# Kernel tuning notes

Hardware: AMD Instinct MI355X
Metric: run time of the kernel (lower is better)

The kernel has to match this reference:

```python
import jax, jax.numpy as jnp
import numpy as np

DIM = 64
WS = 8    # window_size
SS = 4    # shift_size


def _conv(x, w, pad, groups=1):
    return jax.lax.conv_general_dilated(
        x, w, (1, 1), ((pad, pad), (pad, pad)),
        dimension_numbers=('NCHW', 'OIHW', 'NCHW'),
        feature_group_count=groups)


def _window_partition(x, ws):
    # x: (B, C, H, W) -> (B*Hn*Wn, C, ws, ws), with bottom/right padding
    B, C, H, W = x.shape
    pb = (-H) % ws
    pr = (-W) % ws
    x = jnp.pad(x, ((0, 0), (0, 0), (0, pb), (0, pr)))
    Hp, Wp = H + pb, W + pr
    x = x.reshape(B, C, Hp // ws, ws, Wp // ws, ws).transpose(0, 1, 2, 4, 3, 5)
    return x.reshape(-1, C, ws, ws)


def _window_reverse(wins, ws, H, W):
    pb = (-H) % ws
    pr = (-W) % ws
    Hp, Wp = H + pb, W + pr
    B = wins.shape[0] // ((Hp // ws) * (Wp // ws))
    x = wins.reshape(B, -1, Hp // ws, Wp // ws, ws, ws).transpose(0, 1, 2, 4, 3, 5)
    x = x.reshape(B, -1, Hp, Wp)
    return x[:, :, :H, :W]


def _create_mask(H, W, ws, ss):
    # Swin-style additive mask, computed statically with numpy
    Hp = int(np.ceil(H / ws)) * ws
    Wp = int(np.ceil(W / ws)) * ws
    m = np.zeros((Hp, Wp), dtype=np.float32)
    slices = (slice(0, -ws), slice(-ws, -ss), slice(-ss, None))
    cnt = 0
    for hs in slices:
        for wsl in slices:
            m[hs, wsl] = cnt
            cnt += 1
    mw = m.reshape(Hp // ws, ws, Wp // ws, ws).transpose(0, 2, 1, 3).reshape(-1, ws * ws)
    diff = mw[:, None, :] - mw[:, :, None]
    return jnp.asarray(np.where(diff != 0, -100.0, 0.0).astype(np.float32))


def _l2norm(x):
    # matches torch F.normalize(dim=-1, eps=1e-12)
    return x / jnp.maximum(jnp.linalg.norm(x, axis=-1, keepdims=True), 1e-12)


def _win_attn(xw, w_qkv, w_dw, w_proj, ws, mask, b):
    # xw: (N, C, ws, ws) windows
    C = xw.shape[1]
    qkv = _conv(_conv(xw, w_qkv, 0), w_dw, 1, groups=3 * C)
    q, k, v = jnp.split(qkv, 3, axis=1)
    N = q.shape[0]
    hw = ws * ws
    q = _l2norm(q.reshape(N, C, hw))
    k = _l2norm(k.reshape(N, C, hw))
    v = v.reshape(N, C, hw)
    attn = jnp.einsum('nci,ncj->nij', q, k) / ws  # (N, hw, hw)
    if mask is not None:
        attn = (attn.reshape(b, -1, hw, hw) + mask[None]).reshape(-1, hw, hw)
    attn = jax.nn.softmax(attn, axis=-1)
    out = jnp.einsum('nci,nij->ncj', v, attn).reshape(N, C, ws, ws)
    return _conv(out, w_proj, 1)


def _forward(x, w_qkv0, w_dw0, w_proj0, w_qkv1, w_dw1, w_proj1):
    b, c, h, w = x.shape
    # pass 1: unshifted windows
    xw = _window_partition(x, WS)
    out = _win_attn(xw, w_qkv0, w_dw0, w_proj0, WS, None, b)
    out = _window_reverse(out, WS, h, w)
    # pass 2: shifted windows with Swin mask
    shift = jnp.roll(out, (-SS, -SS), axis=(2, 3))
    sw = _window_partition(shift, WS)
    mask = _create_mask(h, w, WS, SS)
    out = _win_attn(sw, w_qkv1, w_dw1, w_proj1, WS, mask, b)
    out = _window_reverse(out, WS, h, w)
    return jnp.roll(out, (SS, SS), axis=(2, 3))


def setup_inputs() -> dict:
    key = jax.random.key(0)
    ks = jax.random.split(key, 7)
    C = DIM
    s = 0.05
    return {
        'x': jax.random.normal(ks[0], (8, C, 256, 256), jnp.float32),
        'w_qkv0': jax.random.normal(ks[1], (3 * C, C, 1, 1), jnp.float32) * s,
        'w_dw0': jax.random.normal(ks[2], (3 * C, 1, 3, 3), jnp.float32) * s,
        'w_proj0': jax.random.normal(ks[3], (C, C, 3, 3), jnp.float32) * s,
        'w_qkv1': jax.random.normal(ks[4], (3 * C, C, 1, 1), jnp.float32) * s,
        'w_dw1': jax.random.normal(ks[5], (3 * C, 1, 3, 3), jnp.float32) * s,
        'w_proj1': jax.random.normal(ks[6], (C, C, 3, 3), jnp.float32) * s,
    }


def reference(x, w_qkv0, w_dw0, w_proj0, w_qkv1, w_dw1, w_proj1):
    return _forward(x, w_qkv0, w_dw0, w_proj0, w_qkv1, w_dw1, w_proj1)
```

## Files before the change

kernel.cpp:

```cpp
#include <hip/hip_runtime.h>


typedef __attribute__((ext_vector_type(8))) short bf8;
typedef __attribute__((ext_vector_type(4))) float f32x4;
#define MFMA(a, b, c) __builtin_amdgcn_mfma_f32_16x16x32_bf16(a, b, c, 0, 0, 0)

__device__ __forceinline__ int xkey(int p) { return ((p >> 3) ^ p) & 7; }
__device__ __forceinline__ int xswz(int p, int c) { return p * 64 + (c ^ (xkey(p) << 3)); }
__device__ __forceinline__ int sswz(int ch, int p) {
    return ch * 64 + (p ^ (((ch >> 1) & 7) << 2));
}
__device__ __forceinline__ int jswz(int ch, int p) {
    return ch * 64 + (p ^ (((ch >> 1) & 7) << 3));
}

__device__ __forceinline__ unsigned cvtpk(float a, float b) {
    unsigned r;
    asm("v_cvt_pk_bf16_f32 %0, %1, %2" : "=v"(r) : "v"(a), "v"(b));
    return r;
}

__device__ __forceinline__ void bsplit(float f, short& h, short& l) {
    unsigned u = __float_as_uint(f);
    unsigned hb = (u + 0x7FFFu + ((u >> 16) & 1u)) >> 16;
    float hf = __uint_as_float(hb << 16);
    float r = f - hf;
    unsigned u2 = __float_as_uint(r);
    unsigned lb = (u2 + 0x7FFFu + ((u2 >> 16) & 1u)) >> 16;
    h = (short)hb; l = (short)lb;
}
__device__ __forceinline__ void bsplit2(float a, float b, unsigned& hw, unsigned& lw) {
    hw = cvtpk(a, b);
    float ra = a - __uint_as_float(hw << 16);
    float rb = b - __uint_as_float(hw & 0xFFFF0000u);
    lw = cvtpk(ra, rb);
}

__global__ void k_fq(const float* __restrict__ wq, short* __restrict__ oh, short* __restrict__ ol) {
    int bx = blockIdx.x;
    int kk = bx / 12, tt = bx % 12;
    int tid = threadIdx.x;
    int lane = tid >> 3, j = tid & 7;
    int oc = tt * 16 + (lane & 15);
    int ic = kk * 32 + ((lane >> 4) << 3) + j;
    short h, l; bsplit(wq[oc * 64 + ic], h, l);
    oh[bx * 512 + tid] = h; ol[bx * 512 + tid] = l;
}
__global__ void k_fp(const float* __restrict__ wp, short* __restrict__ oh, short* __restrict__ ol) {
    int bx = blockIdx.x;
    int tap = bx >> 3, kk = (bx >> 2) & 1, tt = bx & 3;
    int tid = threadIdx.x;
    int lane = tid >> 3, j = tid & 7;
    int oc = tt * 16 + (lane & 15);
    int ic = kk * 32 + ((lane >> 4) << 3) + j;
    short h, l; bsplit(wp[(oc * 64 + ic) * 9 + tap], h, l);
    oh[bx * 512 + tid] = h; ol[bx * 512 + tid] = l;
}

__device__ __forceinline__ void dw_one(const float* scr, const float* wd,
                                       int ch, int row, float o[8]) {
    float w9[9];
    #pragma unroll
    for (int tp = 0; tp < 9; ++tp) w9[tp] = wd[tp];
    float e[3][10];
    #pragma unroll
    for (int k3 = 0; k3 < 3; ++k3) {
        int rr = row - 1 + k3;
        e[k3][0] = 0.f; e[k3][9] = 0.f;
        if ((unsigned)rr < 8u) {
            float4 a = *(const float4*)&scr[sswz(ch, rr * 8)];
            float4 b = *(const float4*)&scr[sswz(ch, rr * 8 + 4)];
            e[k3][1] = a.x; e[k3][2] = a.y; e[k3][3] = a.z; e[k3][4] = a.w;
            e[k3][5] = b.x; e[k3][6] = b.y; e[k3][7] = b.z; e[k3][8] = b.w;
        } else {
            #pragma unroll
            for (int q2 = 1; q2 < 9; ++q2) e[k3][q2] = 0.f;
        }
    }
    #pragma unroll
    for (int s = 0; s < 8; ++s) {
        float a = 0.f;
        #pragma unroll
        for (int k3 = 0; k3 < 3; ++k3)
            #pragma unroll
            for (int dx = 0; dx < 3; ++dx)
                a = fmaf(w9[k3 * 3 + dx], e[k3][s + dx], a);
        o[s] = a;
    }
}

__device__ __forceinline__ float norm8(const float d[8]) {
    float ss = 0.f;
    #pragma unroll
    for (int s = 0; s < 8; ++s) ss = fmaf(d[s], d[s], ss);
    ss += __shfl_xor(ss, 1); ss += __shfl_xor(ss, 2); ss += __shfl_xor(ss, 4);
    return fmaxf(sqrtf(ss), 1e-12f);
}

__device__ __forceinline__ void p2_chunk32(const short* XTh, const short* XTl,
                                           const short* bqh, const short* bql,
                                           float* scr, int chunk,
                                           int mh, int nh, int col, int quad, int qo8, int lane)
{
    f32x4 acc[2];
    #pragma unroll
    for (int mt = 0; mt < 2; ++mt) acc[mt] = (f32x4){0.f, 0.f, 0.f, 0.f};
    #pragma unroll
    for (int kk = 0; kk < 2; ++kk) {
        bf8 Ah[2], Al[2];
        #pragma unroll
        for (int mt = 0; mt < 2; ++mt) {
            int row = (mh * 2 + mt) * 16 + col;
            int ad = row * 64 + ((kk * 32 + qo8) ^ (xkey(row) << 3));
            Ah[mt] = *(const bf8*)&XTh[ad];
            Al[mt] = *(const bf8*)&XTl[ad];
        }
        int tt = chunk * 2 + nh;
        bf8 Bh = *(const bf8*)&bqh[((kk * 12 + tt) * 64 + lane) * 8];
        bf8 Bl = *(const bf8*)&bql[((kk * 12 + tt) * 64 + lane) * 8];
        #pragma unroll
        for (int mt = 0; mt < 2; ++mt) {
            acc[mt] = MFMA(Ah[mt], Bh, acc[mt]);
            acc[mt] = MFMA(Ah[mt], Bl, acc[mt]);
            acc[mt] = MFMA(Al[mt], Bh, acc[mt]);
        }
    }
    #pragma unroll
    for (int mt = 0; mt < 2; ++mt) {
        int ocl = nh * 16 + col;
        int p0 = (mh * 2 + mt) * 16 + quad * 4;
        *(f32x4*)&scr[sswz(ocl, p0)] = acc[mt];
    }
}

__global__ __launch_bounds__(256, 4)
void k_fused(const float* __restrict__ in,
             const short* __restrict__ bqh, const short* __restrict__ bql,
             const float* __restrict__ wdw,
             const short* __restrict__ bph, const short* __restrict__ bpl,
             float* __restrict__ out, int shift, int use_mask, int roll)
{
    __shared__ __align__(16) char smem[40960];
    short* XTh = (short*)smem;
    short* XTl = (short*)(smem + 8192);
    short* kTh = (short*)(smem + 16384);
    short* kTl = (short*)(smem + 24576);
    short* vbh = kTh;
    short* vbl = kTl;
    float* scr = (float*)(smem + 32768);
    short* PTh = (short*)(smem + 32768);
    short* PTl = (short*)(smem + 36864);
    float* projo = (float*)(smem + 16384);

    const int tid = threadIdx.x, lane = tid & 63, wv = tid >> 6;
    const int col = lane & 15, quad = lane >> 4, qo8 = quad * 8;
    const int mh = wv & 1, nh = wv >> 1;
    const int ch = tid >> 3, rrow = tid & 7;
    const int n = blockIdx.x;
    const int b = n >> 10, c = (n >> 4) & 63, t = n & 15;
    const size_t base = ((size_t)(b * 64 + c)) << 16;

    #pragma unroll
    for (int k = 0; k < 16; k += 2) {
        int o0 = tid + k * 256, o1 = o0 + 256;
        int hi0 = o0 >> 11, r0 = (o0 >> 8) & 7, lo0 = (o0 >> 3) & 31, s0 = o0 & 7;
        int hi1 = o1 >> 11, r1 = (o1 >> 8) & 7, lo1 = (o1 >> 3) & 31, s1 = o1 & 7;
        float v0 = in[base + (size_t)(((t * 16 + hi0 * 8 + r0) + shift) & 255) * 256
                           + (((lo0 * 8 + s0) + shift) & 255)];
        float v1 = in[base + (size_t)(((t * 16 + hi1 * 8 + r1) + shift) & 255) * 256
                           + (((lo1 * 8 + s1) + shift) & 255)];
        unsigned hw, lw; bsplit2(v0, v1, hw, lw);
        int ad0 = xswz(r0 * 8 + s0, hi0 * 32 + lo0);
        int ad1 = xswz(r1 * 8 + s1, hi1 * 32 + lo1);
        XTh[ad0] = (short)hw; XTh[ad1] = (short)(hw >> 16);
        XTl[ad0] = (short)lw; XTl[ad1] = (short)(lw >> 16);
    }
    __syncthreads();

    float dqA[8], dqB[8], dvA[8], dvB[8];
    float nqA, nqB;

    p2_chunk32(XTh, XTl, bqh, bql, scr, 0, mh, nh, col, quad, qo8, lane);
    __syncthreads();
    dw_one(scr, wdw + ch * 9, ch, rrow, dqA);
    nqA = norm8(dqA);
    __syncthreads();
    p2_chunk32(XTh, XTl, bqh, bql, scr, 1, mh, nh, col, quad, qo8, lane);
    __syncthreads();
    dw_one(scr, wdw + (32 + ch) * 9, ch, rrow, dqB);
    nqB = norm8(dqB);
    __syncthreads();
    p2_chunk32(XTh, XTl, bqh, bql, scr, 2, mh, nh, col, quad, qo8, lane);
    __syncthreads();
    {
        float dk[8];
        dw_one(scr, wdw + (64 + ch) * 9, ch, rrow, dk);
        float sc = 0.125f / (nqA * norm8(dk));
        #pragma unroll
        for (int s = 0; s < 8; ++s) dk[s] *= sc;
        #pragma unroll
        for (int s0 = 0; s0 < 8; s0 += 2) {
            unsigned hw, lw; bsplit2(dk[s0], dk[s0 + 1], hw, lw);
            int p0 = rrow * 8 + s0;
            int a0 = xswz(p0, ch), a1 = xswz(p0 + 1, ch);
            kTh[a0] = (short)hw; kTh[a1] = (short)(hw >> 16);
            kTl[a0] = (short)lw; kTl[a1] = (short)(lw >> 16);
        }
    }
    __syncthreads();
    p2_chunk32(XTh, XTl, bqh, bql, scr, 3, mh, nh, col, quad, qo8, lane);
    __syncthreads();
    {
        float dk[8];
        dw_one(scr, wdw + (96 + ch) * 9, ch, rrow, dk);
        float sc = 0.125f / (nqB * norm8(dk));
        #pragma unroll
        for (int s = 0; s < 8; ++s) dk[s] *= sc;
        int cg = 32 + ch;
        #pragma unroll
        for (int s0 = 0; s0 < 8; s0 += 2) {
            unsigned hw, lw; bsplit2(dk[s0], dk[s0 + 1], hw, lw);
            int p0 = rrow * 8 + s0;
            int a0 = xswz(p0, cg), a1 = xswz(p0 + 1, cg);
            kTh[a0] = (short)hw; kTh[a1] = (short)(hw >> 16);
            kTl[a0] = (short)lw; kTl[a1] = (short)(lw >> 16);
        }
    }
    __syncthreads();
    p2_chunk32(XTh, XTl, bqh, bql, scr, 4, mh, nh, col, quad, qo8, lane);
    __syncthreads();
    dw_one(scr, wdw + (128 + ch) * 9, ch, rrow, dvA);
    __syncthreads();
    p2_chunk32(XTh, XTl, bqh, bql, scr, 5, mh, nh, col, quad, qo8, lane);
    __syncthreads();
    dw_one(scr, wdw + (160 + ch) * 9, ch, rrow, dvB);
    #pragma unroll
    for (int s0 = 0; s0 < 8; s0 += 2) {
        unsigned hw, lw; bsplit2(dqA[s0], dqA[s0 + 1], hw, lw);
        int p0 = rrow * 8 + s0;
        int a0 = xswz(p0, ch), a1 = xswz(p0 + 1, ch);
        XTh[a0] = (short)hw; XTh[a1] = (short)(hw >> 16);
        XTl[a0] = (short)lw; XTl[a1] = (short)(lw >> 16);
    }
    {
        int cg = 32 + ch;
        #pragma unroll
        for (int s0 = 0; s0 < 8; s0 += 2) {
            unsigned hw, lw; bsplit2(dqB[s0], dqB[s0 + 1], hw, lw);
            int p0 = rrow * 8 + s0;
            int a0 = xswz(p0, cg), a1 = xswz(p0 + 1, cg);
            XTh[a0] = (short)hw; XTh[a1] = (short)(hw >> 16);
            XTl[a0] = (short)lw; XTl[a1] = (short)(lw >> 16);
        }
    }
    __syncthreads();

    f32x4 at[4];
    #pragma unroll
    for (int nt = 0; nt < 4; ++nt) at[nt] = (f32x4){0.f, 0.f, 0.f, 0.f};
    {
        bf8 Ah[2], Al[2];
        #pragma unroll
        for (int kk = 0; kk < 2; ++kk) {
            int row = wv * 16 + col;
            int ad = row * 64 + ((kk * 32 + qo8) ^ (xkey(row) << 3));
            Ah[kk] = *(const bf8*)&XTh[ad];
            Al[kk] = *(const bf8*)&XTl[ad];
        }
        #pragma unroll
        for (int kk = 0; kk < 2; ++kk)
            #pragma unroll
            for (int nt = 0; nt < 4; ++nt) {
                int rowB = nt * 16 + col;
                int ad = rowB * 64 + ((kk * 32 + qo8) ^ (xkey(rowB) << 3));
                bf8 Bh = *(const bf8*)&kTh[ad];
                bf8 Bl = *(const bf8*)&kTl[ad];
                at[nt] = MFMA(Ah[kk], Bh, at[nt]);
                at[nt] = MFMA(Ah[kk], Bl, at[nt]);
                at[nt] = MFMA(Al[kk], Bh, at[nt]);
            }
    }
    if (use_mask) {
        const int widx = n & 1023;
        const int hn_m = widx >> 5, wn_m = widx & 31;
        #pragma unroll
        for (int nt = 0; nt < 4; ++nt) {
            int j = nt * 16 + col;
            int rj = ((hn_m == 31) ? (((j >> 3) < 4) ? 1 : 2) : 0) * 3
                   + ((wn_m == 31) ? (((j & 7) < 4) ? 1 : 2) : 0);
            #pragma unroll
            for (int rg = 0; rg < 4; ++rg) {
                int i = wv * 16 + quad * 4 + rg;
                int ri = ((hn_m == 31) ? (((i >> 3) < 4) ? 1 : 2) : 0) * 3
                       + ((wn_m == 31) ? (((i & 7) < 4) ? 1 : 2) : 0);
                if (ri != rj) at[nt][rg] = at[nt][rg] - 100.f;
            }
        }
    }
    float Pv[4][4];
    #pragma unroll
    for (int rg = 0; rg < 4; ++rg) {
        float m = fmaxf(fmaxf(at[0][rg], at[1][rg]), fmaxf(at[2][rg], at[3][rg]));
        m = fmaxf(m, __shfl_xor(m, 1)); m = fmaxf(m, __shfl_xor(m, 2));
        m = fmaxf(m, __shfl_xor(m, 4)); m = fmaxf(m, __shfl_xor(m, 8));
        float e0 = __expf(at[0][rg] - m), e1 = __expf(at[1][rg] - m);
        float e2 = __expf(at[2][rg] - m), e3 = __expf(at[3][rg] - m);
        float s = e0 + e1 + e2 + e3;
        s += __shfl_xor(s, 1); s += __shfl_xor(s, 2);
        s += __shfl_xor(s, 4); s += __shfl_xor(s, 8);
        float is = 1.0f / s;
        Pv[0][rg] = e0 * is; Pv[1][rg] = e1 * is; Pv[2][rg] = e2 * is; Pv[3][rg] = e3 * is;
    }
    __syncthreads();

    #pragma unroll
    for (int hf = 0; hf < 2; ++hf) {
        const float* dv = hf ? dvB : dvA;
        int cg = hf * 32 + ch;
        unsigned hw[4], lw[4];
        #pragma unroll
        for (int q2 = 0; q2 < 4; ++q2) bsplit2(dv[2 * q2], dv[2 * q2 + 1], hw[q2], lw[q2]);
        int ad = cg * 64 + ((rrow ^ xkey(cg)) << 3);
        *(uint4*)&vbh[ad] = (uint4){hw[0], hw[1], hw[2], hw[3]};
        *(uint4*)&vbl[ad] = (uint4){lw[0], lw[1], lw[2], lw[3]};
    }
    #pragma unroll
    for (int q = 0; q < 2; ++q) {
        int nt = q;
        int jl = q * 16 + col;
        #pragma unroll
        for (int rp = 0; rp < 2; ++rp) {
            unsigned hw, lw; bsplit2(Pv[nt][2 * rp], Pv[nt][2 * rp + 1], hw, lw);
            int i0 = wv * 16 + quad * 4 + 2 * rp;
            int ad = jl * 64 + (i0 ^ (xkey(jl) << 3));
            *(unsigned*)&PTh[ad] = hw; *(unsigned*)&PTl[ad] = lw;
        }
    }
    __syncthreads();

    #pragma unroll
    for (int h = 0; h < 2; ++h) {
        if (h == 1) {
            #pragma unroll
            for (int q = 0; q < 2; ++q) {
                int nt = 2 + q;
                int jl = q * 16 + col;
                #pragma unroll
                for (int rp = 0; rp < 2; ++rp) {
                    unsigned hw, lw; bsplit2(Pv[nt][2 * rp], Pv[nt][2 * rp + 1], hw, lw);
                    int i0 = wv * 16 + quad * 4 + 2 * rp;
                    int ad = jl * 64 + (i0 ^ (xkey(jl) << 3));
                    *(unsigned*)&PTh[ad] = hw; *(unsigned*)&PTl[ad] = lw;
                }
            }
            __syncthreads();
        }
        f32x4 av[2];
        #pragma unroll
        for (int mt = 0; mt < 2; ++mt) av[mt] = (f32x4){0.f, 0.f, 0.f, 0.f};
        #pragma unroll
        for (int kk = 0; kk < 2; ++kk) {
            bf8 Ah[2], Al[2];
            #pragma unroll
            for (int mt = 0; mt < 2; ++mt) {
                int row = (mh * 2 + mt) * 16 + col;
                int ad = row * 64 + ((kk * 32 + qo8) ^ (xkey(row) << 3));
                Ah[mt] = *(const bf8*)&vbh[ad];
                Al[mt] = *(const bf8*)&vbl[ad];
            }
            int jl = nh * 16 + col;
            int bd = jl * 64 + ((kk * 32 + qo8) ^ (xkey(jl) << 3));
            bf8 Bh = *(const bf8*)&PTh[bd];
            bf8 Bl = *(const bf8*)&PTl[bd];
            #pragma unroll
            for (int mt = 0; mt < 2; ++mt) {
                av[mt] = MFMA(Ah[mt], Bh, av[mt]);
                av[mt] = MFMA(Ah[mt], Bl, av[mt]);
                av[mt] = MFMA(Al[mt], Bh, av[mt]);
            }
        }
        int j = (h * 2 + nh) * 16 + col;
        #pragma unroll
        for (int mt = 0; mt < 2; ++mt) {
            int c0 = (mh * 2 + mt) * 16 + quad * 4;
            #pragma unroll
            for (int rp = 0; rp < 2; ++rp) {
                unsigned hw, lw; bsplit2(av[mt][2 * rp], av[mt][2 * rp + 1], hw, lw);
                int ad = j * 64 + ((c0 + 2 * rp) ^ (xkey(j) << 3));
                *(unsigned*)&XTh[ad] = hw;
                *(unsigned*)&XTl[ad] = lw;
            }
        }
        __syncthreads();
    }

    if (tid < 32) ((unsigned*)(smem + 32768))[tid] = 0u;
    __syncthreads();

    {
        f32x4 ap[2][2];
        #pragma unroll
        for (int mt = 0; mt < 2; ++mt)
            #pragma unroll
            for (int nt = 0; nt < 2; ++nt) ap[mt][nt] = (f32x4){0.f, 0.f, 0.f, 0.f};
        const int smc = col & 7;
        #pragma unroll 1
        for (int tap = 0; tap < 9; ++tap) {
            int dy = (tap >= 6) ? 1 : ((tap >= 3) ? 0 : -1);
            int dx = tap - (dy + 1) * 3 - 1;
            int ra_h[2], ra_l[2];
            #pragma unroll
            for (int mt = 0; mt < 2; ++mt) {
                int rr = (mh * 2 + mt) * 2 + (col >> 3) + dy;
                int ss = smc + dx;
                bool ok = ((unsigned)rr < 8u) && ((unsigned)ss < 8u);
                int row = rr * 8 + ss;
                ra_h[mt] = ok ? row : 256;
                ra_l[mt] = ok ? row : 192;
            }
            #pragma unroll
            for (int kk = 0; kk < 2; ++kk) {
                bf8 Bh[2], Bl[2], Ah[2], Al[2];
                #pragma unroll
                for (int nt = 0; nt < 2; ++nt) {
                    int bi = (((tap * 2 + kk) * 4 + (nh * 2 + nt)) * 64 + lane) * 8;
                    Bh[nt] = *(const bf8*)&bph[bi];
                    Bl[nt] = *(const bf8*)&bpl[bi];
                }
                #pragma unroll
                for (int mt = 0; mt < 2; ++mt) {
                    int adh = ra_h[mt] * 64 + ((kk * 32 + qo8) ^ (xkey(ra_h[mt]) << 3));
                    int adl = ra_l[mt] * 64 + ((kk * 32 + qo8) ^ (xkey(ra_l[mt]) << 3));
                    Ah[mt] = *(const bf8*)&XTh[adh];
                    Al[mt] = *(const bf8*)&XTl[adl];
                }
                #pragma unroll
                for (int mt = 0; mt < 2; ++mt)
                    #pragma unroll
                    for (int nt = 0; nt < 2; ++nt) {
                        ap[mt][nt] = MFMA(Ah[mt], Bh[nt], ap[mt][nt]);
                        ap[mt][nt] = MFMA(Ah[mt], Bl[nt], ap[mt][nt]);
                        ap[mt][nt] = MFMA(Al[mt], Bh[nt], ap[mt][nt]);
                    }
            }
        }
        #pragma unroll
        for (int nt = 0; nt < 2; ++nt) {
            int oc = (nh * 2 + nt) * 16 + col;
            #pragma unroll
            for (int mt = 0; mt < 2; ++mt) {
                int p0 = (mh * 2 + mt) * 16 + quad * 4;
                *(f32x4*)&projo[jswz(oc, p0)] = ap[mt][nt];
            }
        }
    }
    __syncthreads();

    #pragma unroll
    for (int k = 0; k < 16; ++k) {
        int o = tid + k * 256;
        int hi = o >> 11, r = (o >> 8) & 7, lo = (o >> 3) & 31, s = o & 7;
        int c2 = hi * 32 + lo;
        float v = projo[jswz(c2, r * 8 + s)];
        int h2 = t * 16 + hi * 8 + r, w2 = lo * 8 + s;
        out[base + (size_t)((h2 + roll) & 255) * 256 + ((w2 + roll) & 255)] = v;
    }
}

extern "C" void kernel_launch(void* const* d_in, const int* in_sizes, int n_in,
                              void* d_out, int out_size, void* d_ws, size_t ws_size,
                              hipStream_t stream)
{
    const float* x      = (const float*)d_in[0];
    const float* wqkv0  = (const float*)d_in[1];
    const float* wdw0   = (const float*)d_in[2];
    const float* wproj0 = (const float*)d_in[3];
    const float* wqkv1  = (const float*)d_in[4];
    const float* wdw1   = (const float*)d_in[5];
    const float* wproj1 = (const float*)d_in[6];
    float* out = (float*)d_out;

    float* tmp = (float*)d_ws;
    short* fb  = (short*)(tmp + 33554432);
    short* bq0h = fb;
    short* bq0l = fb + 12288;
    short* bq1h = fb + 24576;
    short* bq1l = fb + 36864;
    short* bp0h = fb + 49152;
    short* bp0l = fb + 86016;
    short* bp1h = fb + 122880;
    short* bp1l = fb + 159744;

    hipLaunchKernelGGL(k_fq, dim3(24), dim3(512), 0, stream, wqkv0, bq0h, bq0l);
    hipLaunchKernelGGL(k_fq, dim3(24), dim3(512), 0, stream, wqkv1, bq1h, bq1l);
    hipLaunchKernelGGL(k_fp, dim3(72), dim3(512), 0, stream, wproj0, bp0h, bp0l);
    hipLaunchKernelGGL(k_fp, dim3(72), dim3(512), 0, stream, wproj1, bp1h, bp1l);

    hipLaunchKernelGGL(k_fused, dim3(8192), dim3(256), 0, stream,
                       x, bq0h, bq0l, wdw0, bp0h, bp0l, tmp, 0, 0, 0);
    hipLaunchKernelGGL(k_fused, dim3(8192), dim3(256), 0, stream,
                       tmp, bq1h, bq1l, wdw1, bp1h, bp1l, out, 4, 1, 4);
}
```

Before: 624.2 us.

## Shrink fused window-attention LDS to 32KB and raise occupancy to five blocks

The LDS footprint drops from 40KB to 32KB so more workgroups fit per CU, and launch bounds rise from 4 to 5. To make room, the v channels are computed before k, K is split into two half-width swizzled buffers, and the attn·V product is restructured into two K-halves that accumulate over i. The buffers are also aliased differently and an extra barrier is added before the projection output overwrites shared memory. The tighter launch bound may force register spills, and the reordered stages add barriers and keep more values live in registers.

Measured after the change: 962.1 us. 1.54x slower.

```diff
diff --git a/kernel.cpp b/kernel.cpp
--- a/kernel.cpp
+++ b/kernel.cpp
@@ -7,6 +7,9 @@
 
 __device__ __forceinline__ int xkey(int p) { return ((p >> 3) ^ p) & 7; }
 __device__ __forceinline__ int xswz(int p, int c) { return p * 64 + (c ^ (xkey(p) << 3)); }
+__device__ __forceinline__ int kswz(int r, int c) {
+    return r * 32 + (c ^ ((((r >> 3) ^ (r >> 1)) & 3) << 3));
+}
 __device__ __forceinline__ int sswz(int ch, int p) {
     return ch * 64 + (p ^ (((ch >> 1) & 7) << 2));
 }
@@ -133,23 +136,25 @@
     }
 }
 
-__global__ __launch_bounds__(256, 4)
+__global__ __launch_bounds__(256, 5)
 void k_fused(const float* __restrict__ in,
              const short* __restrict__ bqh, const short* __restrict__ bql,
              const float* __restrict__ wdw,
              const short* __restrict__ bph, const short* __restrict__ bpl,
              float* __restrict__ out, int shift, int use_mask, int roll)
 {
-    __shared__ __align__(16) char smem[40960];
+    __shared__ __align__(16) char smem[32768];
     short* XTh = (short*)smem;
     short* XTl = (short*)(smem + 8192);
-    short* kTh = (short*)(smem + 16384);
-    short* kTl = (short*)(smem + 24576);
-    short* vbh = kTh;
-    short* vbl = kTl;
-    float* scr = (float*)(smem + 32768);
-    short* PTh = (short*)(smem + 32768);
-    short* PTl = (short*)(smem + 36864);
+    short* K0h = (short*)(smem + 16384);
+    short* K0l = (short*)(smem + 20480);
+    short* K1h = (short*)(smem + 24576);
+    short* K1l = (short*)(smem + 28672);
+    float* scr = (float*)(smem + 24576);
+    short* vbh = (short*)(smem + 16384);
+    short* vbl = (short*)(smem + 20480);
+    short* PTf = (short*)(smem + 24576);
+    short* PTg = (short*)(smem + 28672);
     float* projo = (float*)(smem + 16384);
 
     const int tid = threadIdx.x, lane = tid & 63, wv = tid >> 6;
@@ -190,6 +195,14 @@
     dw_one(scr, wdw + (32 + ch) * 9, ch, rrow, dqB);
     nqB = norm8(dqB);
     __syncthreads();
+    p2_chunk32(XTh, XTl, bqh, bql, scr, 4, mh, nh, col, quad, qo8, lane);
+    __syncthreads();
+    dw_one(scr, wdw + (128 + ch) * 9, ch, rrow, dvA);
+    __syncthreads();
+    p2_chunk32(XTh, XTl, bqh, bql, scr, 5, mh, nh, col, quad, qo8, lane);
+    __syncthreads();
+    dw_one(scr, wdw + (160 + ch) * 9, ch, rrow, dvB);
+    __syncthreads();
     p2_chunk32(XTh, XTl, bqh, bql, scr, 2, mh, nh, col, quad, qo8, lane);
     __syncthreads();
     {
@@ -202,38 +215,21 @@
         for (int s0 = 0; s0 < 8; s0 += 2) {
             unsigned hw, lw; bsplit2(dk[s0], dk[s0 + 1], hw, lw);
             int p0 = rrow * 8 + s0;
-            int a0 = xswz(p0, ch), a1 = xswz(p0 + 1, ch);
-            kTh[a0] = (short)hw; kTh[a1] = (short)(hw >> 16);
-            kTl[a0] = (short)lw; kTl[a1] = (short)(lw >> 16);
+            int a0 = kswz(p0, ch), a1 = kswz(p0 + 1, ch);
+            K0h[a0] = (short)hw; K0h[a1] = (short)(hw >> 16);
+            K0l[a0] = (short)lw; K0l[a1] = (short)(lw >> 16);
         }
     }
     __syncthreads();
     p2_chunk32(XTh, XTl, bqh, bql, scr, 3, mh, nh, col, quad, qo8, lane);
     __syncthreads();
+    float dk1[8];
+    dw_one(scr, wdw + (96 + ch) * 9, ch, rrow, dk1);
     {
-        float dk[8];
-        dw_one(scr, wdw + (96 + ch) * 9, ch, rrow, dk);
-        float sc = 0.125f / (nqB * norm8(dk));
-        #pragma unroll
-        for (int s = 0; s < 8; ++s) dk[s] *= sc;
-        int cg = 32 + ch;
-        #pragma unroll
-        for (int s0 = 0; s0 < 8; s0 += 2) {
-            unsigned hw, lw; bsplit2(dk[s0], dk[s0 + 1], hw, lw);
-            int p0 = rrow * 8 + s0;
-            int a0 = xswz(p0, cg), a1 = xswz(p0 + 1, cg);
-            kTh[a0] = (short)hw; kTh[a1] = (short)(hw >> 16);
-            kTl[a0] = (short)lw; kTl[a1] = (short)(lw >> 16);
-        }
-    }
-    __syncthreads();
-    p2_chunk32(XTh, XTl, bqh, bql, scr, 4, mh, nh, col, quad, qo8, lane);
-    __syncthreads();
-    dw_one(scr, wdw + (128 + ch) * 9, ch, rrow, dvA);
-    __syncthreads();
-    p2_chunk32(XTh, XTl, bqh, bql, scr, 5, mh, nh, col, quad, qo8, lane);
-    __syncthreads();
-    dw_one(scr, wdw + (160 + ch) * 9, ch, rrow, dvB);
+        float sc = 0.125f / (nqB * norm8(dk1));
+        #pragma unroll
+        for (int s = 0; s < 8; ++s) dk1[s] *= sc;
+    }
     #pragma unroll
     for (int s0 = 0; s0 < 8; s0 += 2) {
         unsigned hw, lw; bsplit2(dqA[s0], dqA[s0 + 1], hw, lw);
@@ -254,6 +250,15 @@
         }
     }
     __syncthreads();
+    #pragma unroll
+    for (int s0 = 0; s0 < 8; s0 += 2) {
+        unsigned hw, lw; bsplit2(dk1[s0], dk1[s0 + 1], hw, lw);
+        int p0 = rrow * 8 + s0;
+        int a0 = kswz(p0, ch), a1 = kswz(p0 + 1, ch);
+        K1h[a0] = (short)hw; K1h[a1] = (short)(hw >> 16);
+        K1l[a0] = (short)lw; K1l[a1] = (short)(lw >> 16);
+    }
+    __syncthreads();
 
     f32x4 at[4];
     #pragma unroll
@@ -268,17 +273,20 @@
             Al[kk] = *(const bf8*)&XTl[ad];
         }
         #pragma unroll
-        for (int kk = 0; kk < 2; ++kk)
+        for (int kk = 0; kk < 2; ++kk) {
+            const short* Bph = kk ? K1h : K0h;
+            const short* Bpl = kk ? K1l : K0l;
             #pragma unroll
             for (int nt = 0; nt < 4; ++nt) {
                 int rowB = nt * 16 + col;
-                int ad = rowB * 64 + ((kk * 32 + qo8) ^ (xkey(rowB) << 3));
-                bf8 Bh = *(const bf8*)&kTh[ad];
-                bf8 Bl = *(const bf8*)&kTl[ad];
+                int ad = kswz(rowB, qo8);
+                bf8 Bh = *(const bf8*)&Bph[ad];
+                bf8 Bl = *(const bf8*)&Bpl[ad];
                 at[nt] = MFMA(Ah[kk], Bh, at[nt]);
                 at[nt] = MFMA(Ah[kk], Bl, at[nt]);
                 at[nt] = MFMA(Al[kk], Bh, at[nt]);
             }
+        }
     }
     if (use_mask) {
         const int widx = n & 1023;
@@ -313,88 +321,85 @@
     }
     __syncthreads();
 
-    #pragma unroll
-    for (int hf = 0; hf < 2; ++hf) {
-        const float* dv = hf ? dvB : dvA;
-        int cg = hf * 32 + ch;
-        unsigned hw[4], lw[4];
-        #pragma unroll
-        for (int q2 = 0; q2 < 4; ++q2) bsplit2(dv[2 * q2], dv[2 * q2 + 1], hw[q2], lw[q2]);
-        int ad = cg * 64 + ((rrow ^ xkey(cg)) << 3);
-        *(uint4*)&vbh[ad] = (uint4){hw[0], hw[1], hw[2], hw[3]};
-        *(uint4*)&vbl[ad] = (uint4){lw[0], lw[1], lw[2], lw[3]};
-    }
-    #pragma unroll
-    for (int q = 0; q < 2; ++q) {
-        int nt = q;
-        int jl = q * 16 + col;
-        #pragma unroll
-        for (int rp = 0; rp < 2; ++rp) {
-            unsigned hw, lw; bsplit2(Pv[nt][2 * rp], Pv[nt][2 * rp + 1], hw, lw);
-            int i0 = wv * 16 + quad * 4 + 2 * rp;
-            int ad = jl * 64 + (i0 ^ (xkey(jl) << 3));
-            *(unsigned*)&PTh[ad] = hw; *(unsigned*)&PTl[ad] = lw;
-        }
-    }
-    __syncthreads();
-
-    #pragma unroll
-    for (int h = 0; h < 2; ++h) {
-        if (h == 1) {
-            #pragma unroll
-            for (int q = 0; q < 2; ++q) {
-                int nt = 2 + q;
-                int jl = q * 16 + col;
+    f32x4 av[2][2];
+    #pragma unroll
+    for (int mt = 0; mt < 2; ++mt)
+        #pragma unroll
+        for (int nt = 0; nt < 2; ++nt) av[mt][nt] = (f32x4){0.f, 0.f, 0.f, 0.f};
+    #pragma unroll
+    for (int ih = 0; ih < 2; ++ih) {
+        if ((rrow >> 2) == ih) {
+            int rl = rrow & 3;
+            #pragma unroll
+            for (int hf = 0; hf < 2; ++hf) {
+                const float* dv = hf ? dvB : dvA;
+                int cg = hf * 32 + ch;
+                unsigned hw[4], lw[4];
+                #pragma unroll
+                for (int q2 = 0; q2 < 4; ++q2)
+                    bsplit2(dv[2 * q2], dv[2 * q2 + 1], hw[q2], lw[q2]);
+                int ad = kswz(cg, rl * 8);
+                *(uint4*)&vbh[ad] = (uint4){hw[0], hw[1], hw[2], hw[3]};
+                *(uint4*)&vbl[ad] = (uint4){lw[0], lw[1], lw[2], lw[3]};
+            }
+        }
+        if ((wv >> 1) == ih) {
+            #pragma unroll
+            for (int nt = 0; nt < 4; ++nt) {
+                int j = nt * 16 + col;
                 #pragma unroll
                 for (int rp = 0; rp < 2; ++rp) {
                     unsigned hw, lw; bsplit2(Pv[nt][2 * rp], Pv[nt][2 * rp + 1], hw, lw);
-                    int i0 = wv * 16 + quad * 4 + 2 * rp;
-                    int ad = jl * 64 + (i0 ^ (xkey(jl) << 3));
-                    *(unsigned*)&PTh[ad] = hw; *(unsigned*)&PTl[ad] = lw;
+                    int il = (wv & 1) * 16 + quad * 4 + 2 * rp;
+                    int ad = kswz(j, il);
+                    *(unsigned*)&PTf[ad] = hw; *(unsigned*)&PTg[ad] = lw;
                 }
             }
-            __syncthreads();
-        }
-        f32x4 av[2];
-        #pragma unroll
-        for (int mt = 0; mt < 2; ++mt) av[mt] = (f32x4){0.f, 0.f, 0.f, 0.f};
-        #pragma unroll
-        for (int kk = 0; kk < 2; ++kk) {
-            bf8 Ah[2], Al[2];
+        }
+        __syncthreads();
+        {
+            bf8 Ah[2], Al[2], Bh[2], Bl[2];
             #pragma unroll
             for (int mt = 0; mt < 2; ++mt) {
                 int row = (mh * 2 + mt) * 16 + col;
-                int ad = row * 64 + ((kk * 32 + qo8) ^ (xkey(row) << 3));
+                int ad = kswz(row, qo8);
                 Ah[mt] = *(const bf8*)&vbh[ad];
                 Al[mt] = *(const bf8*)&vbl[ad];
             }
-            int jl = nh * 16 + col;
-            int bd = jl * 64 + ((kk * 32 + qo8) ^ (xkey(jl) << 3));
-            bf8 Bh = *(const bf8*)&PTh[bd];
-            bf8 Bl = *(const bf8*)&PTl[bd];
-            #pragma unroll
-            for (int mt = 0; mt < 2; ++mt) {
-                av[mt] = MFMA(Ah[mt], Bh, av[mt]);
-                av[mt] = MFMA(Ah[mt], Bl, av[mt]);
-                av[mt] = MFMA(Al[mt], Bh, av[mt]);
-            }
-        }
-        int j = (h * 2 + nh) * 16 + col;
+            #pragma unroll
+            for (int nt = 0; nt < 2; ++nt) {
+                int rowB = (nh * 2 + nt) * 16 + col;
+                int ad = kswz(rowB, qo8);
+                Bh[nt] = *(const bf8*)&PTf[ad];
+                Bl[nt] = *(const bf8*)&PTg[ad];
+            }
+            #pragma unroll
+            for (int mt = 0; mt < 2; ++mt)
+                #pragma unroll
+                for (int nt = 0; nt < 2; ++nt) {
+                    av[mt][nt] = MFMA(Ah[mt], Bh[nt], av[mt][nt]);
+                    av[mt][nt] = MFMA(Ah[mt], Bl[nt], av[mt][nt]);
+                    av[mt][nt] = MFMA(Al[mt], Bh[nt], av[mt][nt]);
+                }
+        }
+        __syncthreads();
+    }
+    #pragma unroll
+    for (int nt = 0; nt < 2; ++nt) {
+        int j = (nh * 2 + nt) * 16 + col;
         #pragma unroll
         for (int mt = 0; mt < 2; ++mt) {
             int c0 = (mh * 2 + mt) * 16 + quad * 4;
             #pragma unroll
             for (int rp = 0; rp < 2; ++rp) {
-                unsigned hw, lw; bsplit2(av[mt][2 * rp], av[mt][2 * rp + 1], hw, lw);
+                unsigned hw, lw; bsplit2(av[mt][nt][2 * rp], av[mt][nt][2 * rp + 1], hw, lw);
                 int ad = j * 64 + ((c0 + 2 * rp) ^ (xkey(j) << 3));
                 *(unsigned*)&XTh[ad] = hw;
                 *(unsigned*)&XTl[ad] = lw;
             }
         }
-        __syncthreads();
-    }
-
-    if (tid < 32) ((unsigned*)(smem + 32768))[tid] = 0u;
+    }
+    if (tid < 32) ((unsigned*)(smem + 16384))[tid] = 0u;
     __syncthreads();
 
     {
@@ -415,8 +420,8 @@
                 int ss = smc + dx;
                 bool ok = ((unsigned)rr < 8u) && ((unsigned)ss < 8u);
                 int row = rr * 8 + ss;
-                ra_h[mt] = ok ? row : 256;
-                ra_l[mt] = ok ? row : 192;
+                ra_h[mt] = ok ? row : 128;
+                ra_l[mt] = ok ? row : 64;
             }
             #pragma unroll
             for (int kk = 0; kk < 2; ++kk) {
@@ -444,6 +449,7 @@
                     }
             }
         }
+        __syncthreads();
         #pragma unroll
         for (int nt = 0; nt < 2; ++nt) {
             int oc = (nh * 2 + nt) * 16 + col;
```
